# Kernel optimization log

Measured on AMD Instinct MI355X. Metric: run time of the kernel, lower is better.

Reference implementation:

```python
import jax, jax.numpy as jnp
import numpy as np

N_QUBITS = 12
N_LAYERS = 3


def _apply_ry(state, theta, q):
    # state: (2,)*n real statevector; RY on qubit q
    c = jnp.cos(theta * 0.5)
    s = jnp.sin(theta * 0.5)
    st = jnp.moveaxis(state, q, 0)
    st = jnp.stack([c * st[0] - s * st[1], s * st[0] + c * st[1]])
    return jnp.moveaxis(st, 0, q)


def _apply_cz(state, q, r):
    st = jnp.moveaxis(state, (q, r), (0, 1))
    st = st.at[1, 1].multiply(-1.0)
    return jnp.moveaxis(st, (0, 1), (q, r))


def _embed(x, params):
    # angle-embedding ansatz: L layers of RY(theta[l,q]+x[q]) + CZ ring
    n = N_QUBITS
    state = jnp.zeros((2,) * n, dtype=x.dtype).at[(0,) * n].set(1.0)
    for l in range(N_LAYERS):
        for q in range(n):
            state = _apply_ry(state, params[l, q] + x[q], q)
        for q in range(n):
            state = _apply_cz(state, q, (q + 1) % n)
    return state.reshape(-1)  # (2^n,)


def setup_inputs() -> dict:
    key = jax.random.key(0)
    k1, k2, k3 = jax.random.split(key, 3)
    data = jax.random.uniform(k1, (2048, N_QUBITS), dtype=jnp.float32)
    labels = jax.random.randint(k2, (2048,), 0, 2, dtype=jnp.int32)
    params = jax.random.normal(k3, (N_LAYERS, N_QUBITS), dtype=jnp.float32)
    return {"data": data, "labels": labels, "params": params}


def reference(data, labels, params):
    # Psi[i] = U(x_i, params)|0>, k_ij = |<psi_j|psi_i>|^2 (== prob of amp 0 of U^dag(x_j)U(x_i)|0>)
    psi = jax.vmap(_embed, in_axes=(0, None))(data, params)  # (N, 2^n)
    K = jnp.square(psi @ psi.T)                              # (N, N) pairwise kernel
    lab = 2.0 * labels.astype(psi.dtype) - 1.0               # {0,1} -> {-1,+1}
    LL = jnp.outer(lab, lab)
    kernel_polarity = jnp.sum(LL * K)
    square_sum_k = jnp.sum(K * K)
    square_sum_l = jnp.sum(LL * LL)
    return kernel_polarity / jnp.sqrt(square_sum_k * square_sum_l)
```

## Files before the change

### kernel.cpp

```cpp
#include <hip/hip_runtime.h>
#include <math.h>

#define NQ    12
#define DIM   4096
#define K_EXT 8192
#define KSL   1024
#define NSAMP 2048
#define NLAY  3
#define NT2   16
#define NTRI2 136
#define NSLICE 8
#define BK    64

typedef __attribute__((ext_vector_type(8)))  short bf16x8;
typedef __attribute__((ext_vector_type(16))) float floatx16;

__device__ __forceinline__ unsigned short f32_to_bf16(float x) {
    unsigned u = __builtin_bit_cast(unsigned, x);
    u += 0x7FFFu + ((u >> 16) & 1u);
    return (unsigned short)(u >> 16);
}
__device__ __forceinline__ float bf16_to_f32(unsigned short h) {
    unsigned u = (unsigned)h << 16;
    return __builtin_bit_cast(float, u);
}

__device__ __forceinline__ void gl_lds16(const unsigned short* g, unsigned short* l) {
    __builtin_amdgcn_global_load_lds(
        (const __attribute__((address_space(1))) unsigned int*)g,
        (__attribute__((address_space(3))) unsigned int*)l,
        16, 0, 0);
}

__device__ __forceinline__ void tri_decode(int bid, int& bi, int& bj) {
    int i = (int)((33.0 - sqrt(33.0*33.0 - 8.0*(double)bid)) * 0.5);
    int start = i*(33-i)/2;
    while (bid < start)               { --i; start = i*(33-i)/2; }
    while (bid >= start + (NT2 - i))  { start += NT2 - i; ++i; }
    bi = i; bj = i + (bid - start);
}

__global__ __launch_bounds__(256) void sim_kernel(const float* __restrict__ data,
                                                  const float* __restrict__ params,
                                                  unsigned short* __restrict__ pe)
{
    __shared__ float CS[2*36], SN[2*36];
    __shared__ float trans[2][4608];
    const int tid  = threadIdx.x;
    const int wave = tid >> 6, lane = tid & 63;
    const int sidx = wave >> 1;
    const int w    = wave & 1;
    const int smp  = blockIdx.x * 2 + sidx;

    if (w == 0 && lane < NLAY*NQ) {
        const int q = lane % NQ;
        const float th = 0.5f * (params[lane] + data[smp*NQ + q]);
        CS[sidx*36 + lane] = cosf(th);
        SN[sidx*36 + lane] = sinf(th);
    }
    __syncthreads();

    float v[32];
    #pragma unroll
    for (int r = 0; r < 32; ++r) v[r] = 0.f;
    if (w == 0 && lane == 0) v[0] = 1.f;

    float* buf = trans[sidx];
    float* wb  = buf + 36*lane + 2304*w;
    const float* rb = buf + ((lane>>2)&15) + 16*w + 36*(lane&3);

    #pragma unroll 1
    for (int l = 0; l < NLAY; ++l) {
        const float* cs = &CS[sidx*36 + l*NQ];
        const float* sn = &SN[sidx*36 + l*NQ];
        const int even = !(l & 1);

        {
            const int qb = even ? 7 : 2;
            #pragma unroll
            for (int b = 0; b < 5; ++b) {
                const float c = cs[qb + b], s = sn[qb + b];
                const int M = 1 << b;
                #pragma unroll
                for (int r = 0; r < 32; ++r) {
                    if (!(r & M)) {
                        const float a0 = v[r], a1 = v[r | M];
                        v[r]     = c * a0 - s * a1;
                        v[r | M] = s * a0 + c * a1;
                    }
                }
            }
        }
        {
            const float c0 = cs[0], s0 = sn[0];
            const float t0 = (lane & 1) ? s0 : -s0;
            #pragma unroll
            for (int r = 0; r < 32; ++r) {
                const int iv = __builtin_bit_cast(int, v[r]);
                const int pv = __builtin_amdgcn_update_dpp(0, iv, 0xB1, 0xF, 0xF, true);
                v[r] = c0 * v[r] + t0 * __builtin_bit_cast(float, pv);
            }
            const float c1 = cs[1], s1 = sn[1];
            const float t1 = (lane & 2) ? s1 : -s1;
            #pragma unroll
            for (int r = 0; r < 32; ++r) {
                const int iv = __builtin_bit_cast(int, v[r]);
                const int pv = __builtin_amdgcn_update_dpp(0, iv, 0x4E, 0xF, 0xF, true);
                v[r] = c1 * v[r] + t1 * __builtin_bit_cast(float, pv);
            }
        }
        __syncthreads();
        #pragma unroll
        for (int t = 0; t < 8; ++t) {
            float4 q4;
            q4.x = v[4*t]; q4.y = v[4*t+1]; q4.z = v[4*t+2]; q4.w = v[4*t+3];
            *(float4*)&wb[4*t] = q4;
        }
        __syncthreads();
        #pragma unroll
        for (int r = 0; r < 32; ++r)
            v[r] = rb[144*(r & 15) + 2304*(r >> 4)];

        {
            const int qb = even ? 2 : 7;
            #pragma unroll
            for (int b = 0; b < 5; ++b) {
                const float c = cs[qb + b], s = sn[qb + b];
                const int M = 1 << b;
                #pragma unroll
                for (int r = 0; r < 32; ++r) {
                    if (!(r & M)) {
                        const float a0 = v[r], a1 = v[r | M];
                        v[r]     = c * a0 - s * a1;
                        v[r | M] = s * a0 + c * a1;
                    }
                }
            }
        }
        {
            const int Base = even ? ((lane & 3) | (((lane >> 2) & 15) << 7) | (w << 11))
                                  : (lane | (w << 6));
            const int shift = even ? 2 : 7;
            #pragma unroll
            for (int r = 0; r < 32; ++r) {
                const int i  = Base | (r << shift);
                const int t  = ((i >> 1) | (i << 11)) & 0xFFF;
                const int p  = __popc(i & t) & 1;
                v[r] = __builtin_bit_cast(float, __builtin_bit_cast(int, v[r]) ^ (p << 31));
            }
        }
    }

    const int sw = smp & 7;
    const int ell = w*64 + lane;
    unsigned short* outb = pe + (size_t)smp * K_EXT;
    #pragma unroll
    for (int c = 0; c < 4; ++c) {
        uint4 H, L;
        {
            const float x0 = v[c*8+0], x1 = v[c*8+1];
            const unsigned short h0 = f32_to_bf16(x0), h1 = f32_to_bf16(x1);
            H.x = (unsigned)h0 | ((unsigned)h1 << 16);
            L.x = (unsigned)f32_to_bf16(x0 - bf16_to_f32(h0)) |
                  ((unsigned)f32_to_bf16(x1 - bf16_to_f32(h1)) << 16);
        }
        {
            const float x0 = v[c*8+2], x1 = v[c*8+3];
            const unsigned short h0 = f32_to_bf16(x0), h1 = f32_to_bf16(x1);
            H.y = (unsigned)h0 | ((unsigned)h1 << 16);
            L.y = (unsigned)f32_to_bf16(x0 - bf16_to_f32(h0)) |
                  ((unsigned)f32_to_bf16(x1 - bf16_to_f32(h1)) << 16);
        }
        {
            const float x0 = v[c*8+4], x1 = v[c*8+5];
            const unsigned short h0 = f32_to_bf16(x0), h1 = f32_to_bf16(x1);
            H.z = (unsigned)h0 | ((unsigned)h1 << 16);
            L.z = (unsigned)f32_to_bf16(x0 - bf16_to_f32(h0)) |
                  ((unsigned)f32_to_bf16(x1 - bf16_to_f32(h1)) << 16);
        }
        {
            const float x0 = v[c*8+6], x1 = v[c*8+7];
            const unsigned short h0 = f32_to_bf16(x0), h1 = f32_to_bf16(x1);
            H.w = (unsigned)h0 | ((unsigned)h1 << 16);
            L.w = (unsigned)f32_to_bf16(x0 - bf16_to_f32(h0)) |
                  ((unsigned)f32_to_bf16(x1 - bf16_to_f32(h1)) << 16);
        }
        const int gc  = 4*ell + c;
        const int pos = (gc & ~7) | ((gc ^ sw) & 7);
        *(uint4*)&outb[pos*8]       = H;
        *(uint4*)&outb[DIM + pos*8] = L;
    }
}

__global__ __launch_bounds__(256) void gram_partial(const unsigned short* __restrict__ pe,
                                                    float* __restrict__ Gp)
{
    __shared__ __align__(16) unsigned short stage[2*128*64];

    unsigned short* As = stage;
    unsigned short* Bs = stage + 128*64;

    const int tid   = threadIdx.x;
    const int tile  = blockIdx.x >> 3;
    const int slice = blockIdx.x & 7;
    int bi, bj; tri_decode(tile, bi, bj);
    const int k0 = slice * KSL;

    const int wave = tid >> 6, lane = tid & 63;
    const int qr = (wave >> 1) * 64;
    const int qc = (wave &  1) * 64;
    const int mrow = lane & 31;
    const int chsel = lane >> 5;
    const int sw = mrow & 7;

    floatx16 c00, c01, c10, c11;
    #pragma unroll
    for (int i = 0; i < 16; ++i) { c00[i]=0.f; c01[i]=0.f; c10[i]=0.f; c11[i]=0.f; }

    const int mat  = wave >> 1;
    const int half = wave & 1;
    const unsigned short* gbase = pe
        + ((size_t)((mat ? bj : bi)*128 + half*64 + (lane >> 3))) * K_EXT
        + k0 + (lane & 7)*8;
    unsigned short* lbase = (mat ? Bs : As) + half*64*64;

    for (int kk = 0; kk < KSL; kk += BK) {
        __syncthreads();
        const unsigned short* g = gbase + kk;
        #pragma unroll
        for (int i = 0; i < 8; ++i)
            gl_lds16(g + (size_t)i*8*K_EXT, lbase + i*512);
        __syncthreads();

        #pragma unroll
        for (int ks = 0; ks < 4; ++ks) {
            const int ch = (ks*2 + chsel) ^ sw;
            const bf16x8 a0 = *(const bf16x8*)&As[(qr +      mrow)*64 + ch*8];
            const bf16x8 a1 = *(const bf16x8*)&As[(qr + 32 + mrow)*64 + ch*8];
            const bf16x8 b0 = *(const bf16x8*)&Bs[(qc +      mrow)*64 + ch*8];
            const bf16x8 b1 = *(const bf16x8*)&Bs[(qc + 32 + mrow)*64 + ch*8];
            c00 = __builtin_amdgcn_mfma_f32_32x32x16_bf16(a0, b0, c00, 0, 0, 0);
            c01 = __builtin_amdgcn_mfma_f32_32x32x16_bf16(a0, b1, c01, 0, 0, 0);
            c10 = __builtin_amdgcn_mfma_f32_32x32x16_bf16(a1, b0, c10, 0, 0, 0);
            c11 = __builtin_amdgcn_mfma_f32_32x32x16_bf16(a1, b1, c11, 0, 0, 0);
        }
    }

    float* Gt = Gp + ((size_t)slice * NTRI2 + tile) * 16384;
    const int crow = chsel * 4;
    const int ccol = lane & 31;
    #pragma unroll
    for (int rr = 0; rr < 16; ++rr) {
        const int rl = (rr & 3) + 8*(rr >> 2) + crow;
        const int r0 = qr + rl,  r1 = qr + 32 + rl;
        const int cA = qc + ccol, cB = qc + 32 + ccol;
        Gt[r0*128 + cA] = c00[rr];
        Gt[r0*128 + cB] = c01[rr];
        Gt[r1*128 + cA] = c10[rr];
        Gt[r1*128 + cB] = c11[rr];
    }
}

__global__ __launch_bounds__(256) void gram_reduce(const float* __restrict__ Gp,
                                                   const int* __restrict__ labels,
                                                   double* __restrict__ part1,
                                                   double* __restrict__ part2)
{
    __shared__ float la[128], lb[128];
    __shared__ double red[256];
    const int tid  = threadIdx.x;
    const int tile = blockIdx.x >> 2;
    const int quar = blockIdx.x & 3;
    int bi, bj; tri_decode(tile, bi, bj);

    if (tid < 128) la[tid]       = 2.0f*(float)labels[bi*128 + tid]       - 1.0f;
    else           lb[tid - 128] = 2.0f*(float)labels[bj*128 + tid - 128] - 1.0f;
    __syncthreads();

    const size_t stride = (size_t)NTRI2 * 16384;
    const float* g0 = Gp + (size_t)tile * 16384 + quar * 4096;

    double s1 = 0.0, s2 = 0.0;
    #pragma unroll 2
    for (int u = 0; u < 16; ++u) {
        const int e  = u*256 + tid;
        const int ge = quar*4096 + e;
        float g = 0.f;
        #pragma unroll
        for (int s = 0; s < NSLICE; ++s) g += g0[e + (size_t)s*stride];
        const int row = ge >> 7, col = ge & 127;
        const float w = (bi < bj) ? 2.0f : ((row < col) ? 2.0f : ((row == col) ? 1.0f : 0.0f));
        const float g2 = g * g;
        s1 += (double)(w * la[row] * lb[col] * g2);
        const double d = (double)g2;
        s2 += (double)w * d * d;
    }

    red[tid] = s1; __syncthreads();
    for (int off = 128; off; off >>= 1) { if (tid < off) red[tid] += red[tid+off]; __syncthreads(); }
    if (tid == 0) part1[blockIdx.x] = red[0];
    __syncthreads();
    red[tid] = s2; __syncthreads();
    for (int off = 128; off; off >>= 1) { if (tid < off) red[tid] += red[tid+off]; __syncthreads(); }
    if (tid == 0) part2[blockIdx.x] = red[0];
}

__global__ __launch_bounds__(256) void finalize_kernel(const double* __restrict__ part1,
                                                       const double* __restrict__ part2,
                                                       float* __restrict__ out)
{
    __shared__ double r1[256], r2[256];
    const int tid = threadIdx.x;
    double a = 0.0, b = 0.0;
    #pragma unroll
    for (int u = 0; u < 3; ++u) {
        const int s = tid + u*256;
        if (s < NTRI2*4) { a += part1[s]; b += part2[s]; }
    }
    r1[tid] = a; r2[tid] = b; __syncthreads();
    for (int off = 128; off; off >>= 1) {
        if (tid < off) { r1[tid] += r1[tid+off]; r2[tid] += r2[tid+off]; }
        __syncthreads();
    }
    if (tid == 0) out[0] = (float)(r1[0] / (sqrt(r2[0]) * (double)NSAMP));
}

extern "C" void kernel_launch(void* const* d_in, const int* in_sizes, int n_in,
                              void* d_out, int out_size, void* d_ws, size_t ws_size,
                              hipStream_t stream)
{
    const float* data   = (const float*)d_in[0];
    const int*   labels = (const int*)d_in[1];
    const float* params = (const float*)d_in[2];

    double* part1 = (double*)d_ws;
    double* part2 = part1 + 768;
    unsigned short* psi_ext = (unsigned short*)((char*)d_ws + 16384);
    float* Gp = (float*)((char*)d_ws + 16384 + (size_t)NSAMP*K_EXT*2);

    sim_kernel<<<NSAMP/2, 256, 0, stream>>>(data, params, psi_ext);
    gram_partial<<<NTRI2*NSLICE, 256, 0, stream>>>(psi_ext, Gp);
    gram_reduce<<<NTRI2*4, 256, 0, stream>>>(Gp, labels, part1, part2);
    finalize_kernel<<<1, 256, 0, stream>>>(part1, part2, (float*)d_out);
}
```

Baseline: 149.8 us.

## Double-buffer LDS staging and use 2 waves with 128x64 warp tiles in gram_partial

```diff
diff --git a/kernel.cpp b/kernel.cpp
--- a/kernel.cpp
+++ b/kernel.cpp
@@ -192,13 +192,42 @@
     }
 }
 
-__global__ __launch_bounds__(256) void gram_partial(const unsigned short* __restrict__ pe,
+__device__ __forceinline__ void stage16(const unsigned short* __restrict__ g,
+                                        unsigned short* __restrict__ l)
+{
+    #pragma unroll
+    for (int i = 0; i < 16; ++i)
+        gl_lds16(g + (size_t)i*8*K_EXT, l + i*512);
+}
+
+__device__ __forceinline__ void compute64(const unsigned short* __restrict__ A,
+                                          const unsigned short* __restrict__ B,
+                                          int mrow, int chsel, int sw, int wv,
+                                          floatx16 (&c)[4][2])
+{
+    #pragma unroll
+    for (int ks = 0; ks < 4; ++ks) {
+        const int ch = (ks*2 + chsel) ^ sw;
+        bf16x8 a[4], b[2];
+        #pragma unroll
+        for (int R = 0; R < 4; ++R)
+            a[R] = *(const bf16x8*)&A[(R*32 + mrow)*64 + ch*8];
+        #pragma unroll
+        for (int cb = 0; cb < 2; ++cb)
+            b[cb] = *(const bf16x8*)&B[(wv*64 + cb*32 + mrow)*64 + ch*8];
+        #pragma unroll
+        for (int R = 0; R < 4; ++R) {
+            #pragma unroll
+            for (int cb = 0; cb < 2; ++cb)
+                c[R][cb] = __builtin_amdgcn_mfma_f32_32x32x16_bf16(a[R], b[cb], c[R][cb], 0, 0, 0);
+        }
+    }
+}
+
+__global__ __launch_bounds__(128) void gram_partial(const unsigned short* __restrict__ pe,
                                                     float* __restrict__ Gp)
 {
-    __shared__ __align__(16) unsigned short stage[2*128*64];
-
-    unsigned short* As = stage;
-    unsigned short* Bs = stage + 128*64;
+    __shared__ __align__(16) unsigned short stage[2][2*128*64];
 
     const int tid   = threadIdx.x;
     const int tile  = blockIdx.x >> 3;
@@ -206,58 +235,52 @@
     int bi, bj; tri_decode(tile, bi, bj);
     const int k0 = slice * KSL;
 
-    const int wave = tid >> 6, lane = tid & 63;
-    const int qr = (wave >> 1) * 64;
-    const int qc = (wave &  1) * 64;
-    const int mrow = lane & 31;
+    const int wv    = tid >> 6;
+    const int lane  = tid & 63;
+    const int mrow  = lane & 31;
     const int chsel = lane >> 5;
-    const int sw = mrow & 7;
-
-    floatx16 c00, c01, c10, c11;
-    #pragma unroll
-    for (int i = 0; i < 16; ++i) { c00[i]=0.f; c01[i]=0.f; c10[i]=0.f; c11[i]=0.f; }
-
-    const int mat  = wave >> 1;
-    const int half = wave & 1;
+    const int sw    = mrow & 7;
+
+    floatx16 c[4][2];
+    #pragma unroll
+    for (int R = 0; R < 4; ++R)
+        #pragma unroll
+        for (int cb = 0; cb < 2; ++cb)
+            #pragma unroll
+            for (int i = 0; i < 16; ++i) c[R][cb][i] = 0.f;
+
     const unsigned short* gbase = pe
-        + ((size_t)((mat ? bj : bi)*128 + half*64 + (lane >> 3))) * K_EXT
+        + ((size_t)((wv ? bj : bi)*128 + (lane >> 3))) * K_EXT
         + k0 + (lane & 7)*8;
-    unsigned short* lbase = (mat ? Bs : As) + half*64*64;
-
-    for (int kk = 0; kk < KSL; kk += BK) {
+    const int sofs = wv ? 8192 : 0;
+
+    stage16(gbase, &stage[0][sofs]);
+    __syncthreads();
+
+    int cur = 0;
+    #pragma unroll 1
+    for (int kk = 0; kk < KSL - BK; kk += BK) {
+        stage16(gbase + kk + BK, &stage[cur ^ 1][sofs]);
+        compute64(&stage[cur][0], &stage[cur][8192], mrow, chsel, sw, wv, c);
         __syncthreads();
-        const unsigned short* g = gbase + kk;
-        #pragma unroll
-        for (int i = 0; i < 8; ++i)
-            gl_lds16(g + (size_t)i*8*K_EXT, lbase + i*512);
-        __syncthreads();
-
-        #pragma unroll
-        for (int ks = 0; ks < 4; ++ks) {
-            const int ch = (ks*2 + chsel) ^ sw;
-            const bf16x8 a0 = *(const bf16x8*)&As[(qr +      mrow)*64 + ch*8];
-            const bf16x8 a1 = *(const bf16x8*)&As[(qr + 32 + mrow)*64 + ch*8];
-            const bf16x8 b0 = *(const bf16x8*)&Bs[(qc +      mrow)*64 + ch*8];
-            const bf16x8 b1 = *(const bf16x8*)&Bs[(qc + 32 + mrow)*64 + ch*8];
-            c00 = __builtin_amdgcn_mfma_f32_32x32x16_bf16(a0, b0, c00, 0, 0, 0);
-            c01 = __builtin_amdgcn_mfma_f32_32x32x16_bf16(a0, b1, c01, 0, 0, 0);
-            c10 = __builtin_amdgcn_mfma_f32_32x32x16_bf16(a1, b0, c10, 0, 0, 0);
-            c11 = __builtin_amdgcn_mfma_f32_32x32x16_bf16(a1, b1, c11, 0, 0, 0);
-        }
-    }
+        cur ^= 1;
+    }
+    compute64(&stage[cur][0], &stage[cur][8192], mrow, chsel, sw, wv, c);
 
     float* Gt = Gp + ((size_t)slice * NTRI2 + tile) * 16384;
+    const int ccol = lane & 31;
     const int crow = chsel * 4;
-    const int ccol = lane & 31;
-    #pragma unroll
-    for (int rr = 0; rr < 16; ++rr) {
-        const int rl = (rr & 3) + 8*(rr >> 2) + crow;
-        const int r0 = qr + rl,  r1 = qr + 32 + rl;
-        const int cA = qc + ccol, cB = qc + 32 + ccol;
-        Gt[r0*128 + cA] = c00[rr];
-        Gt[r0*128 + cB] = c01[rr];
-        Gt[r1*128 + cA] = c10[rr];
-        Gt[r1*128 + cB] = c11[rr];
+    #pragma unroll
+    for (int R = 0; R < 4; ++R) {
+        #pragma unroll
+        for (int cb = 0; cb < 2; ++cb) {
+            const int col = wv*64 + cb*32 + ccol;
+            #pragma unroll
+            for (int rr = 0; rr < 16; ++rr) {
+                const int rl = (rr & 3) + 8*(rr >> 2) + crow;
+                Gt[(R*32 + rl)*128 + col] = c[R][cb][rr];
+            }
+        }
     }
 }
 
@@ -339,7 +362,7 @@
     float* Gp = (float*)((char*)d_ws + 16384 + (size_t)NSAMP*K_EXT*2);
 
     sim_kernel<<<NSAMP/2, 256, 0, stream>>>(data, params, psi_ext);
-    gram_partial<<<NTRI2*NSLICE, 256, 0, stream>>>(psi_ext, Gp);
+    gram_partial<<<NTRI2*NSLICE, 128, 0, stream>>>(psi_ext, Gp);
     gram_reduce<<<NTRI2*4, 256, 0, stream>>>(Gp, labels, part1, part2);
     finalize_kernel<<<1, 256, 0, stream>>>(part1, part2, (float*)d_out);
 }
```

Result: slower. 156.0 us (+4.2%).
